# Optimization experiments

Hardware: AMD Instinct MI355X
Metric: run time of the kernel (lower is better)

## Reference

```python
import jax, jax.numpy as jnp
import numpy as np

N_SEQ, BS, E, H = 2048, 8, 512, 8
HD = E // H  # 64


def setup_inputs() -> dict:
    key = jax.random.key(0)
    k1, k2, k3 = jax.random.split(key, 3)
    seq = jax.random.normal(k1, (N_SEQ, BS, E), dtype=jnp.float32)
    # xavier_uniform for Linear(E, 3E): bound = sqrt(6/(fan_in+fan_out))
    b_qkv_w = float(np.sqrt(6.0 / (E + 3 * E)))
    W_qkv = jax.random.uniform(k2, (3 * E, E), minval=-b_qkv_w, maxval=b_qkv_w, dtype=jnp.float32)
    b_out_w = float(np.sqrt(6.0 / (E + E)))
    W_out = jax.random.uniform(k3, (E, E), minval=-b_out_w, maxval=b_out_w, dtype=jnp.float32)
    b_qkv = jnp.zeros((3 * E,), dtype=jnp.float32)
    b_out = jnp.zeros((E,), dtype=jnp.float32)
    return {"seq": seq, "W_qkv": W_qkv, "b_qkv": b_qkv, "W_out": W_out, "b_out": b_out}


def reference(seq, W_qkv, b_qkv, W_out, b_out):
    n, bs, e = seq.shape
    # fused QKV projection: [n, bs, 3E]
    qkv = jnp.einsum('nbe,fe->nbf', seq, W_qkv) + b_qkv
    # [n, bs, 3, H, HD] -> q/k/v each [n, bs*H, HD] (bs outer, H inner)
    qkv = qkv.reshape(n, bs, 3, H, HD)
    q = qkv[:, :, 0].reshape(n, bs * H, HD)
    k = qkv[:, :, 1].reshape(n, bs * H, HD)
    v = qkv[:, :, 2].reshape(n, bs * H, HD)
    scale = 1.0 / jnp.sqrt(jnp.asarray(HD, dtype=seq.dtype))
    # full [bs*H, n, n] score matrix as in the original
    attn = jnp.einsum('qbd,kbd->bqk', q * scale, k)
    attn = jax.nn.softmax(attn, axis=-1)
    out = jnp.einsum('bqk,kbd->qbd', attn, v)  # [n, bs*H, HD]
    out = out.reshape(n, bs, e)
    return jnp.einsum('nbe,fe->nbf', out, W_out) + b_out
```

## Files before the change

### kernel.cpp

```cpp
#include <hip/hip_runtime.h>
#include <stdint.h>

typedef unsigned short ushort_t;
typedef unsigned int uint32;
typedef __attribute__((ext_vector_type(8))) short short8;
typedef __attribute__((ext_vector_type(4))) float f32x4;
typedef __attribute__((ext_vector_type(16))) float f32x16;
typedef __attribute__((ext_vector_type(4))) uint32 uint4v;

#define NSEQ 2048
#define BSZ 8
#define EMB 512
#define NHEAD 8
#define HDIM 64
#define MTOK (NSEQ*BSZ)
#define NH_TOT (BSZ*NHEAD)
#define NT (NSEQ/64)

#define VMCNT0 asm volatile("s_waitcnt vmcnt(0)" ::: "memory")
#define BAR __builtin_amdgcn_s_barrier()

__device__ __forceinline__ ushort_t f2bf(float f) {
  uint32_t u = __builtin_bit_cast(uint32_t, f);
  u += 0x7FFFu + ((u >> 16) & 1u);
  return (ushort_t)(u >> 16);
}
__device__ __forceinline__ float bf2f(ushort_t u) {
  uint32_t x = ((uint32_t)u) << 16;
  return __builtin_bit_cast(float, x);
}

__device__ __forceinline__ void gll16(const void* g, void* l) {
  __builtin_amdgcn_global_load_lds(
      (const __attribute__((address_space(1))) void*)g,
      (__attribute__((address_space(3))) void*)l, 16, 0, 0);
}

__device__ __forceinline__ int SW(int r) { return (r & 7) ^ ((r >> 3) & 7); }

__global__ void cvt_f32_bf16(const float* __restrict__ in, ushort_t* __restrict__ out, int n4) {
  int i = blockIdx.x * blockDim.x + threadIdx.x;
  if (i >= n4) return;
  float4 v = reinterpret_cast<const float4*>(in)[i];
  union { ushort_t u[4]; uint64_t q; } o;
  o.u[0] = f2bf(v.x); o.u[1] = f2bf(v.y); o.u[2] = f2bf(v.z); o.u[3] = f2bf(v.w);
  reinterpret_cast<uint64_t*>(out)[i] = o.q;
}

template<int MODE>
__global__ __launch_bounds__(256) void gemm_bt(
    const ushort_t* __restrict__ A, const ushort_t* __restrict__ B,
    const float* __restrict__ bias,
    float* __restrict__ Cf, ushort_t* __restrict__ Cq,
    int M, int N, int K)
{
  __shared__ __align__(16) ushort_t As[128*64];
  __shared__ __align__(16) ushort_t Bs[128*64];
  const int t = threadIdx.x;
  const int w = t >> 6, l = t & 63;
  const int tm = blockIdx.y * 128, tn = blockIdx.x * 128;
  const int wm = w >> 1, wn = w & 1;

  f32x4 acc[4][4] = {};

  for (int k0 = 0; k0 < K; k0 += 64) {
    #pragma unroll
    for (int j = 0; j < 4; ++j) {
      int row = j*32 + w*8 + (l >> 3);
      int cole = ((l & 7) * 8) ^ ((row & 7) << 3);
      const ushort_t* ga = A + (size_t)(tm + row) * K + k0 + cole;
      const ushort_t* gb = B + (size_t)(tn + row) * K + k0 + cole;
      gll16(ga, As + j*2048 + w*512 + l*8);
      gll16(gb, Bs + j*2048 + w*512 + l*8);
    }
    __syncthreads();
    #pragma unroll
    for (int kk = 0; kk < 2; ++kk) {
      short8 af[4], bfr[4];
      #pragma unroll
      for (int mi = 0; mi < 4; ++mi) {
        int row = wm*64 + mi*16 + (l & 15);
        int byte = row*128 + ((kk*64 + ((l >> 4) * 16)) ^ ((row & 7) << 4));
        af[mi] = *reinterpret_cast<const short8*>(reinterpret_cast<const char*>(As) + byte);
      }
      #pragma unroll
      for (int ni = 0; ni < 4; ++ni) {
        int row = wn*64 + ni*16 + (l & 15);
        int byte = row*128 + ((kk*64 + ((l >> 4) * 16)) ^ ((row & 7) << 4));
        bfr[ni] = *reinterpret_cast<const short8*>(reinterpret_cast<const char*>(Bs) + byte);
      }
      #pragma unroll
      for (int mi = 0; mi < 4; ++mi)
        #pragma unroll
        for (int ni = 0; ni < 4; ++ni)
          acc[mi][ni] = __builtin_amdgcn_mfma_f32_16x16x32_bf16(af[mi], bfr[ni], acc[mi][ni], 0, 0, 0);
    }
    __syncthreads();
  }

  #pragma unroll
  for (int mi = 0; mi < 4; ++mi) {
    #pragma unroll
    for (int ni = 0; ni < 4; ++ni) {
      #pragma unroll
      for (int r = 0; r < 4; ++r) {
        int row = tm + wm*64 + mi*16 + ((l >> 4) * 4) + r;
        int col = tn + wn*64 + ni*16 + (l & 15);
        float v = acc[mi][ni][r] + bias[col];
        if constexpr (MODE == 1) {
          Cf[(size_t)row * N + col] = v;
        } else {
          int w3 = col >> 9, hx = (col >> 6) & 7, hd = col & 63;
          int n = row >> 3, bb = row & 7;
          Cq[(size_t)w3 * ((size_t)NH_TOT * NSEQ * HDIM)
             + ((size_t)(bb * NHEAD + hx) * NSEQ + n) * HDIM + hd] = f2bf(v);
        }
      }
    }
  }
}

__global__ __launch_bounds__(256) void transpose_v(
    const ushort_t* __restrict__ V, ushort_t* __restrict__ VT)
{
  __shared__ __align__(16) ushort_t T[64*64];
  const int t = threadIdx.x;
  const int head = blockIdx.y;
  const int n0 = blockIdx.x * 64;
  const size_t base = (size_t)head * NSEQ * HDIM;
  const int r = t >> 3, c0 = (t & 7) * 8;

  short8 a = *reinterpret_cast<const short8*>(V + base + (size_t)(n0 + r) * HDIM + c0);
  short8 b = *reinterpret_cast<const short8*>(V + base + (size_t)(n0 + r + 32) * HDIM + c0);
  #pragma unroll
  for (int e = 0; e < 8; ++e) {
    int d = c0 + e; int sw = SW(d) << 4;
    *reinterpret_cast<ushort_t*>(reinterpret_cast<char*>(T) + d*128 + ((r*2) ^ sw)) = (ushort_t)a[e];
    *reinterpret_cast<ushort_t*>(reinterpret_cast<char*>(T) + d*128 + (((r+32)*2) ^ sw)) = (ushort_t)b[e];
  }
  __syncthreads();
  #pragma unroll
  for (int i = 0; i < 2; ++i) {
    int d = (t >> 3) + 32*i, ch = t & 7;
    short8 v = *reinterpret_cast<const short8*>(
        reinterpret_cast<const char*>(T) + d*128 + ((ch*16) ^ (SW(d) << 4)));
    *reinterpret_cast<short8*>(VT + (size_t)head * HDIM * NSEQ + (size_t)d * NSEQ + n0 + ch*8) = v;
  }
}

#define CSC 0.18033688011112042f

__global__ __launch_bounds__(256) void attn_fwd(
    const ushort_t* __restrict__ Qb, const ushort_t* __restrict__ Kb,
    const ushort_t* __restrict__ VTb, ushort_t* __restrict__ Ob)
{
  __shared__ __align__(16) ushort_t Ks[2][64*64];
  __shared__ __align__(16) ushort_t Vs[2][64*64];
  const int t = threadIdx.x, w = t >> 6, l = t & 63;
  const int lq = l & 31, h = l >> 5;
  const int L = blockIdx.x + 16 * blockIdx.y;
  const int Tid = (L & 7) * 128 + (L >> 3);
  const int bh = Tid >> 4, qt = Tid & 15;
  const int b = bh >> 3, hh = bh & 7;
  const size_t hbase  = (size_t)bh * NSEQ * HDIM;
  const size_t vtbase = (size_t)bh * HDIM * NSEQ;
  const int qbase = qt*128 + w*32;

  short8 qreg[4];
  #pragma unroll
  for (int kd = 0; kd < 4; ++kd) {
    short8 raw = *reinterpret_cast<const short8*>(
        Qb + hbase + (size_t)(qbase + lq) * HDIM + kd*16 + h*8);
    short8 q;
    #pragma unroll
    for (int e = 0; e < 8; ++e)
      q[e] = (short)f2bf(bf2f((ushort_t)raw[e]) * CSC);
    qreg[kd] = q;
  }

  f32x16 Oacc[2] = {};
  f32x16 lacc = {};

  const short ONE = (short)0x3F80;
  short8 ones = { ONE, ONE, ONE, ONE, ONE, ONE, ONE, ONE };

  const int srow = t >> 3;
  const int scol = (t & 7) * 8;
  const int c0 = scol ^ (SW(srow) << 3);
  const int c1 = scol ^ (SW(srow + 32) << 3);
  const ushort_t* Kg0 = Kb  + hbase  + (size_t)srow       * HDIM + c0;
  const ushort_t* Kg1 = Kb  + hbase  + (size_t)(srow+32)  * HDIM + c1;
  const ushort_t* Vg0 = VTb + vtbase + (size_t)srow       * NSEQ + c0;
  const ushort_t* Vg1 = VTb + vtbase + (size_t)(srow+32)  * NSEQ + c1;

  auto STAGE = [&](int bi, int kt) {
    size_t ko = (size_t)kt * 64 * HDIM;
    int    vo = kt * 64;
    gll16(Kg0 + ko, &Ks[bi][0]    + t*8);
    gll16(Kg1 + ko, &Ks[bi][2048] + t*8);
    gll16(Vg0 + vo, &Vs[bi][0]    + t*8);
    gll16(Vg1 + vo, &Vs[bi][2048] + t*8);
  };

  STAGE(0, 0);
  VMCNT0; BAR;

  #pragma unroll 1
  for (int kt = 0; kt < NT; ++kt) {
    const int cur = kt & 1;
    if (kt + 1 < NT) STAGE(cur ^ 1, kt + 1);

    const char* KsC = reinterpret_cast<const char*>(&Ks[cur][0]);
    const char* VsC = reinterpret_cast<const char*>(&Vs[cur][0]);

    f32x16 s0 = {}, s1 = {};
    #pragma unroll
    for (int kd = 0; kd < 4; ++kd) {
      short8 kf0 = *reinterpret_cast<const short8*>(
          KsC + lq*128 + ((kd*32 + h*16) ^ (SW(lq) << 4)));
      s0 = __builtin_amdgcn_mfma_f32_32x32x16_bf16(kf0, qreg[kd], s0, 0, 0, 0);
      short8 kf1 = *reinterpret_cast<const short8*>(
          KsC + (32+lq)*128 + ((kd*32 + h*16) ^ (SW(32+lq) << 4)));
      s1 = __builtin_amdgcn_mfma_f32_32x32x16_bf16(kf1, qreg[kd], s1, 0, 0, 0);
    }

    #pragma unroll
    for (int r = 0; r < 16; ++r) {
      s0[r] = __builtin_amdgcn_exp2f(s0[r]);
      s1[r] = __builtin_amdgcn_exp2f(s1[r]);
    }

    uint32 w0[8], w1[8];
    #pragma unroll
    for (int i = 0; i < 8; ++i) {
      float a0 = s0[2*i], b0 = s0[2*i+1];
      float a1 = s1[2*i], b1 = s1[2*i+1];
      asm("v_cvt_pk_bf16_f32 %0, %1, %2" : "=v"(w0[i]) : "v"(a0), "v"(b0));
      asm("v_cvt_pk_bf16_f32 %0, %1, %2" : "=v"(w1[i]) : "v"(a1), "v"(b1));
    }
    uint32 pa[4][4];
    #pragma unroll
    for (int sg = 0; sg < 2; ++sg) {
      uint32 a, bb;
      a = w0[4*sg+0]; bb = w0[4*sg+2];
      asm("v_permlane32_swap_b32 %0, %1" : "+v"(a), "+v"(bb));
      pa[sg][0] = a; pa[sg][2] = bb;
      a = w0[4*sg+1]; bb = w0[4*sg+3];
      asm("v_permlane32_swap_b32 %0, %1" : "+v"(a), "+v"(bb));
      pa[sg][1] = a; pa[sg][3] = bb;
      a = w1[4*sg+0]; bb = w1[4*sg+2];
      asm("v_permlane32_swap_b32 %0, %1" : "+v"(a), "+v"(bb));
      pa[2+sg][0] = a; pa[2+sg][2] = bb;
      a = w1[4*sg+1]; bb = w1[4*sg+3];
      asm("v_permlane32_swap_b32 %0, %1" : "+v"(a), "+v"(bb));
      pa[2+sg][1] = a; pa[2+sg][3] = bb;
    }

    #pragma unroll
    for (int km = 0; km < 4; ++km) {
      uint4v u; u[0] = pa[km][0]; u[1] = pa[km][1]; u[2] = pa[km][2]; u[3] = pa[km][3];
      short8 paf = __builtin_bit_cast(short8, u);
      #pragma unroll
      for (int dt = 0; dt < 2; ++dt) {
        int d = dt*32 + lq;
        short8 vf = *reinterpret_cast<const short8*>(
            VsC + d*128 + ((km*32 + h*16) ^ (SW(d) << 4)));
        Oacc[dt] = __builtin_amdgcn_mfma_f32_32x32x16_bf16(paf, vf, Oacc[dt], 0, 0, 0);
      }
      lacc = __builtin_amdgcn_mfma_f32_32x32x16_bf16(paf, ones, lacc, 0, 0, 0);
    }

    if (kt + 1 < NT) { VMCNT0; BAR; }
  }

  #pragma unroll
  for (int r = 0; r < 16; ++r) {
    float li = __builtin_amdgcn_rcpf(lacc[r]);
    int qrow = (r & 3) + 8*(r >> 2) + 4*h;
    int n = qbase + qrow;
    #pragma unroll
    for (int dt = 0; dt < 2; ++dt) {
      int d = dt*32 + lq;
      Ob[((size_t)n * BSZ + b) * EMB + hh*64 + d] = f2bf(Oacc[dt][r] * li);
    }
  }
}

extern "C" void kernel_launch(void* const* d_in, const int* in_sizes, int n_in,
                              void* d_out, int out_size, void* d_ws, size_t ws_size,
                              hipStream_t stream) {
  (void)in_sizes; (void)n_in; (void)out_size; (void)ws_size;
  const float* seq  = (const float*)d_in[0];
  const float* Wqkv = (const float*)d_in[1];
  const float* bqkv = (const float*)d_in[2];
  const float* Wout = (const float*)d_in[3];
  const float* bout = (const float*)d_in[4];
  float* out = (float*)d_out;

  ushort_t* seq_bf  = (ushort_t*)d_ws;
  ushort_t* wqkv_bf = seq_bf  + (size_t)MTOK * EMB;
  ushort_t* wout_bf = wqkv_bf + (size_t)3 * EMB * EMB;
  ushort_t* qkvbuf  = wout_bf + (size_t)EMB * EMB;
  ushort_t* vtbuf   = qkvbuf  + (size_t)3 * NH_TOT * NSEQ * HDIM;
  ushort_t* attno   = qkvbuf  + (size_t)2 * NH_TOT * NSEQ * HDIM;

  cvt_f32_bf16<<<(MTOK*EMB/4 + 255)/256, 256, 0, stream>>>(seq, seq_bf, MTOK*EMB/4);
  cvt_f32_bf16<<<(3*EMB*EMB/4 + 255)/256, 256, 0, stream>>>(Wqkv, wqkv_bf, 3*EMB*EMB/4);
  cvt_f32_bf16<<<(EMB*EMB/4 + 255)/256, 256, 0, stream>>>(Wout, wout_bf, EMB*EMB/4);

  gemm_bt<0><<<dim3(12, 128), 256, 0, stream>>>(seq_bf, wqkv_bf, bqkv, nullptr, qkvbuf,
                                                MTOK, 3*EMB, EMB);

  const ushort_t* Qb  = qkvbuf;
  const ushort_t* Kb  = qkvbuf + (size_t)NH_TOT * NSEQ * HDIM;
  const ushort_t* Vb  = Kb     + (size_t)NH_TOT * NSEQ * HDIM;

  transpose_v<<<dim3(32, 64), 256, 0, stream>>>(Vb, vtbuf);

  attn_fwd<<<dim3(16, 64), 256, 0, stream>>>(Qb, Kb, vtbuf, attno);

  gemm_bt<1><<<dim3(4, 128), 256, 0, stream>>>(attno, wout_bf, bout, out, nullptr,
                                               MTOK, EMB, EMB);
}
```

Baseline: 182.3 us.

## Triple-buffer K/V tiles with partial vmcnt waits and batched LDS fragment loads

Moves the attention loop from double to triple buffering of K and V tiles in LDS, prefetching two tiles ahead. The wait becomes a partial vmcnt(4), so the next tile's loads stay in flight while the current tile is computed. K and V fragments are now read from LDS in batches ahead of their MFMAs, and setprio raises wave priority around the MFMA blocks. The cost is 48KB of LDS per block instead of 32KB and more registers, which could lower occupancy. A launch-bounds hint of 3 blocks is added to guard against that.

```diff
diff --git a/kernel.cpp b/kernel.cpp
--- a/kernel.cpp
+++ b/kernel.cpp
@@ -18,6 +18,7 @@
 #define NT (NSEQ/64)
 
 #define VMCNT0 asm volatile("s_waitcnt vmcnt(0)" ::: "memory")
+#define VMCNT4 asm volatile("s_waitcnt vmcnt(4)" ::: "memory")
 #define BAR __builtin_amdgcn_s_barrier()
 
 __device__ __forceinline__ ushort_t f2bf(float f) {
@@ -150,12 +151,12 @@
 
 #define CSC 0.18033688011112042f
 
-__global__ __launch_bounds__(256) void attn_fwd(
+__global__ __launch_bounds__(256, 3) void attn_fwd(
     const ushort_t* __restrict__ Qb, const ushort_t* __restrict__ Kb,
     const ushort_t* __restrict__ VTb, ushort_t* __restrict__ Ob)
 {
-  __shared__ __align__(16) ushort_t Ks[2][64*64];
-  __shared__ __align__(16) ushort_t Vs[2][64*64];
+  __shared__ __align__(16) ushort_t Ks[3][64*64];
+  __shared__ __align__(16) ushort_t Vs[3][64*64];
   const int t = threadIdx.x, w = t >> 6, l = t & 63;
   const int lq = l & 31, h = l >> 5;
   const int L = blockIdx.x + 16 * blockIdx.y;
@@ -202,26 +203,52 @@
     gll16(Vg1 + vo, &Vs[bi][2048] + t*8);
   };
 
+  VMCNT0;
   STAGE(0, 0);
-  VMCNT0; BAR;
-
+  STAGE(1, 1);
+
+  int cur = 0;
   #pragma unroll 1
   for (int kt = 0; kt < NT; ++kt) {
-    const int cur = kt & 1;
-    if (kt + 1 < NT) STAGE(cur ^ 1, kt + 1);
+    if (kt + 1 < NT) { VMCNT4; } else { VMCNT0; }
+    BAR;
+    if (kt + 2 < NT) {
+      int sb = cur + 2; if (sb >= 3) sb -= 3;
+      STAGE(sb, kt + 2);
+    }
 
     const char* KsC = reinterpret_cast<const char*>(&Ks[cur][0]);
     const char* VsC = reinterpret_cast<const char*>(&Vs[cur][0]);
 
+    short8 kf[2][4];
+    #pragma unroll
+    for (int rp = 0; rp < 2; ++rp) {
+      int row = rp*32 + lq;
+      int swr = SW(row) << 4;
+      #pragma unroll
+      for (int kd = 0; kd < 4; ++kd)
+        kf[rp][kd] = *reinterpret_cast<const short8*>(
+            KsC + row*128 + ((kd*32 + h*16) ^ swr));
+    }
+
     f32x16 s0 = {}, s1 = {};
+    __builtin_amdgcn_s_setprio(1);
     #pragma unroll
     for (int kd = 0; kd < 4; ++kd) {
-      short8 kf0 = *reinterpret_cast<const short8*>(
-          KsC + lq*128 + ((kd*32 + h*16) ^ (SW(lq) << 4)));
-      s0 = __builtin_amdgcn_mfma_f32_32x32x16_bf16(kf0, qreg[kd], s0, 0, 0, 0);
-      short8 kf1 = *reinterpret_cast<const short8*>(
-          KsC + (32+lq)*128 + ((kd*32 + h*16) ^ (SW(32+lq) << 4)));
-      s1 = __builtin_amdgcn_mfma_f32_32x32x16_bf16(kf1, qreg[kd], s1, 0, 0, 0);
+      s0 = __builtin_amdgcn_mfma_f32_32x32x16_bf16(kf[0][kd], qreg[kd], s0, 0, 0, 0);
+      s1 = __builtin_amdgcn_mfma_f32_32x32x16_bf16(kf[1][kd], qreg[kd], s1, 0, 0, 0);
+    }
+    __builtin_amdgcn_s_setprio(0);
+
+    short8 vf[2][4];
+    #pragma unroll
+    for (int dt = 0; dt < 2; ++dt) {
+      int d = dt*32 + lq;
+      int swd = SW(d) << 4;
+      #pragma unroll
+      for (int km = 0; km < 4; ++km)
+        vf[dt][km] = *reinterpret_cast<const short8*>(
+            VsC + d*128 + ((km*32 + h*16) ^ swd));
     }
 
     #pragma unroll
@@ -256,21 +283,18 @@
       pa[2+sg][1] = a; pa[2+sg][3] = bb;
     }
 
+    __builtin_amdgcn_s_setprio(1);
     #pragma unroll
     for (int km = 0; km < 4; ++km) {
       uint4v u; u[0] = pa[km][0]; u[1] = pa[km][1]; u[2] = pa[km][2]; u[3] = pa[km][3];
       short8 paf = __builtin_bit_cast(short8, u);
-      #pragma unroll
-      for (int dt = 0; dt < 2; ++dt) {
-        int d = dt*32 + lq;
-        short8 vf = *reinterpret_cast<const short8*>(
-            VsC + d*128 + ((km*32 + h*16) ^ (SW(d) << 4)));
-        Oacc[dt] = __builtin_amdgcn_mfma_f32_32x32x16_bf16(paf, vf, Oacc[dt], 0, 0, 0);
-      }
-      lacc = __builtin_amdgcn_mfma_f32_32x32x16_bf16(paf, ones, lacc, 0, 0, 0);
-    }
-
-    if (kt + 1 < NT) { VMCNT0; BAR; }
+      Oacc[0] = __builtin_amdgcn_mfma_f32_32x32x16_bf16(paf, vf[0][km], Oacc[0], 0, 0, 0);
+      Oacc[1] = __builtin_amdgcn_mfma_f32_32x32x16_bf16(paf, vf[1][km], Oacc[1], 0, 0, 0);
+      lacc    = __builtin_amdgcn_mfma_f32_32x32x16_bf16(paf, ones,     lacc,    0, 0, 0);
+    }
+    __builtin_amdgcn_s_setprio(0);
+
+    cur = cur + 1; if (cur >= 3) cur = 0;
   }
 
   #pragma unroll
```

After: 173.5 us. 4.8% less time.
